# Kernel tuning notes

Measured on AMD Instinct MI355X. Metric: run time of the kernel, lower is better.

Reference implementation:

```python
import jax, jax.numpy as jnp
import numpy as np

N_NODES = 50000
N_EDGES = 800000
K_HOPS = 3


def setup_inputs() -> dict:
    key = jax.random.key(0)
    ks = jax.random.split(key, 8)
    x = jax.random.normal(ks[0], (N_NODES, 56), dtype=jnp.float32)
    edge_index = jax.random.randint(ks[1], (2, N_EDGES), 0, N_NODES, dtype=jnp.int64)
    def glorot(k, shape):
        fan_in, fan_out = shape
        s = (6.0 / (fan_in + fan_out)) ** 0.5
        return jax.random.uniform(k, shape, jnp.float32, -s, s)
    return {
        "x": x,
        "edge_index": edge_index,
        "W1": glorot(ks[2], (56, 64)), "b1": jnp.zeros((64,), jnp.float32),
        "W2": glorot(ks[3], (64, 64)), "b2": jnp.zeros((64,), jnp.float32),
        "W3": glorot(ks[4], (64, 64)), "b3": jnp.zeros((64,), jnp.float32),
        "W4": glorot(ks[5], (64, 256)), "b4": jnp.zeros((256,), jnp.float32),
    }


def _gcn_norm(edge_index, num_nodes, dtype):
    # add self loops (PyG SGConv default), then symmetric D^{-1/2}(A+I)D^{-1/2} weights
    loop = jnp.arange(num_nodes, dtype=edge_index.dtype)
    src = jnp.concatenate([edge_index[0], loop])
    dst = jnp.concatenate([edge_index[1], loop])
    deg = jax.ops.segment_sum(jnp.ones_like(src, dtype=dtype), dst, num_segments=num_nodes)
    dinv = jnp.where(deg > 0, jax.lax.rsqrt(deg), 0.0).astype(dtype)
    norm = dinv[src] * dinv[dst]  # [E + N]
    return src, dst, norm


def _propagate_k(h, src, dst, norm, num_nodes, k):
    # k hops of sparse gather-scale-scatter: h <- A_hat @ h
    for _ in range(k):
        h = jax.ops.segment_sum(h[src] * norm[:, None], dst, num_segments=num_nodes)
    return h


def reference(x, edge_index, W1, b1, W2, b2, W3, b3, W4, b4):
    n = x.shape[0]
    src, dst, norm = _gcn_norm(edge_index, n, x.dtype)
    # SGConv layers (dropout is identity in eval mode)
    h = _propagate_k(x, src, dst, norm, n, K_HOPS) @ W1 + b1
    h = _propagate_k(h, src, dst, norm, n, K_HOPS) @ W2 + b2
    h = _propagate_k(h, src, dst, norm, n, K_HOPS) @ W3 + b3
    return h @ W4 + b4  # [N, output]
```

## Files before the change

### kernel.cpp

```cpp
#include <hip/hip_runtime.h>

#define N_NODES 50000
#define N_EDGES 800000
#define N_GROUPS 12500
#define HALF_G 6250
#define GSLOTS 128
#define F_IN 56
#define F_PAD 64
#define F_OUT 256
#define NB 16
#define SEG_SZ 6250
#define ZROW N_NODES
#define PAD_E 0x7FFFFFFF


__global__ __launch_bounds__(256) void k_fill(const int* __restrict__ ei,
                                              int* __restrict__ gcnt,
                                              int* __restrict__ ellg) {
  int seg = blockIdx.x & 7;
  int chunk = blockIdx.x >> 3;
  int nchunks = gridDim.x >> 3;
  int stride = nchunks * blockDim.x;
  for (int e = chunk * blockDim.x + threadIdx.x; e < N_EDGES; e += stride) {
    int d = ei[N_EDGES + e];
    if (d / SEG_SZ == seg) {
      int s = ei[e];
      int g = d >> 2;
      int pos = atomicAdd(&gcnt[g], 1);
      ellg[(g << 7) + pos] = (s << 2) | (d & 3);
    }
  }
}


__global__ void k_self(int* __restrict__ gcnt, int* __restrict__ ellg) {
  int i = blockIdx.x * blockDim.x + threadIdx.x;
  if (i >= N_NODES) return;
  int g = i >> 2;
  int pos = atomicAdd(&gcnt[g], 1);
  ellg[(g << 7) + pos] = (i << 2) | (i & 3);
}


__global__ __launch_bounds__(256) void k_sort(const int* __restrict__ gcnt,
                                              int* __restrict__ ellg,
                                              float* __restrict__ dinv,
                                              float* __restrict__ ideg,
                                              float* __restrict__ sqd) {
  int w = (blockIdx.x * blockDim.x + threadIdx.x) >> 6;
  int l = threadIdx.x & 63;
  int cnt = __builtin_amdgcn_readfirstlane(gcnt[w]);
  int* base = ellg + ((size_t)w << 7);
  int v0 = (l < cnt) ? base[l] : PAD_E;
  int v1 = (64 + l < cnt) ? base[64 + l] : PAD_E;

#pragma unroll
  for (int k = 2; k <= 128; k <<= 1) {
#pragma unroll
    for (int j = 64; j > 0; j >>= 1) {
      if (j >= k) continue;
      if (j == 64) {
        int lo = min(v0, v1), hi = max(v0, v1);
        v0 = lo; v1 = hi;
      } else {
        int o0 = __shfl_xor(v0, j);
        int o1 = __shfl_xor(v1, j);
        bool lower = ((l & j) == 0);
        bool up0 = ((l & k) == 0);
        bool up1 = (((l + 64) & k) == 0);
        v0 = (lower == up0) ? min(v0, o0) : max(v0, o0);
        v1 = (lower == up1) ? min(v1, o1) : max(v1, o1);
      }
    }
  }

  int c0 = __popcll(__ballot(v0 != PAD_E && (v0 & 3) == 0)) +
           __popcll(__ballot(v1 != PAD_E && (v1 & 3) == 0));
  int c1 = __popcll(__ballot(v0 != PAD_E && (v0 & 3) == 1)) +
           __popcll(__ballot(v1 != PAD_E && (v1 & 3) == 1));
  int c2 = __popcll(__ballot(v0 != PAD_E && (v0 & 3) == 2)) +
           __popcll(__ballot(v1 != PAD_E && (v1 & 3) == 2));
  int c3 = __popcll(__ballot(v0 != PAD_E && (v0 & 3) == 3)) +
           __popcll(__ballot(v1 != PAD_E && (v1 & 3) == 3));
  if (l < 4) {
    int c = (l == 0) ? c0 : (l == 1) ? c1 : (l == 2) ? c2 : c3;
    float fc = (float)c;
    int node = (w << 2) + l;
    dinv[node] = rsqrtf(fc);
    ideg[node] = 1.0f / fc;
    sqd[node]  = sqrtf(fc);
  }

  base[l] = (v0 == PAD_E) ? (ZROW << 2) : v0;
  base[64 + l] = (v1 == PAD_E) ? (ZROW << 2) : v1;
}


__global__ void k_loadx(const float* __restrict__ x, const float* __restrict__ dinv,
                        float* __restrict__ h) {
  int i = blockIdx.x * blockDim.x + threadIdx.x;
  int nn = i >> 6, f = i & 63;
  float di = dinv[nn];
  float v = 0.f;
  if (f < F_IN) v = x[nn * F_IN + f] * di;
  else if (f == F_IN) v = di;
  h[i] = v;
}


template<bool ASC>
__device__ __forceinline__ void hop_group(int g, const float* __restrict__ hin,
                                          float* __restrict__ hout,
                                          const int* __restrict__ gcnt,
                                          const int* __restrict__ ellg,
                                          const float* __restrict__ ideg,
                                          float* __restrict__ vsave,
                                          int lane, int sub, int m, int fo) {
  int cnt = __builtin_amdgcn_readfirstlane(gcnt[g]);
  const int* base = ellg + ((size_t)g << 7);
  int rec0 = base[lane];
  int rec1 = base[64 + lane];
  float4 acc0 = make_float4(0.f, 0.f, 0.f, 0.f);
  float4 acc1 = acc0, acc2 = acc0, acc3 = acc0;
  int nq = (cnt + 3) >> 2;

#define GATHER(QI, EV, AV)                                                \
  int idx_##EV = ((QI) << 2) + sub;                                       \
  int EV = (idx_##EV < 64) ? __shfl(rec0, idx_##EV)                       \
                           : __shfl(rec1, idx_##EV - 64);                 \
  float4 AV = *(const float4*)(hin + (((size_t)(EV >> 2)) << 6) + fo);

#define ACCUM(EV, AV) {                                                   \
    int dd = EV & 3;                                                      \
    float m0 = (dd == 0) ? 1.f : 0.f;                                     \
    float m1 = (dd == 1) ? 1.f : 0.f;                                     \
    float m2 = (dd == 2) ? 1.f : 0.f;                                     \
    float m3 = (dd == 3) ? 1.f : 0.f;                                     \
    acc0.x = fmaf(m0, AV.x, acc0.x); acc0.y = fmaf(m0, AV.y, acc0.y);     \
    acc0.z = fmaf(m0, AV.z, acc0.z); acc0.w = fmaf(m0, AV.w, acc0.w);     \
    acc1.x = fmaf(m1, AV.x, acc1.x); acc1.y = fmaf(m1, AV.y, acc1.y);     \
    acc1.z = fmaf(m1, AV.z, acc1.z); acc1.w = fmaf(m1, AV.w, acc1.w);     \
    acc2.x = fmaf(m2, AV.x, acc2.x); acc2.y = fmaf(m2, AV.y, acc2.y);     \
    acc2.z = fmaf(m2, AV.z, acc2.z); acc2.w = fmaf(m2, AV.w, acc2.w);     \
    acc3.x = fmaf(m3, AV.x, acc3.x); acc3.y = fmaf(m3, AV.y, acc3.y);     \
    acc3.z = fmaf(m3, AV.z, acc3.z); acc3.w = fmaf(m3, AV.w, acc3.w);     \
  }

  int it = 0;
  for (; it + 2 <= nq; it += 2) {
    int q0 = ASC ? it : (nq - 1 - it);
    int q1 = ASC ? (it + 1) : (nq - 2 - it);
    GATHER(q0, e0, a0)
    GATHER(q1, e1, a1)
    ACCUM(e0, a0)
    ACCUM(e1, a1)
  }
  if (it < nq) {
    int q0 = ASC ? it : (nq - 1 - it);
    GATHER(q0, e0, a0)
    ACCUM(e0, a0)
  }
#undef GATHER
#undef ACCUM

#define RED(A) \
  A.x += __shfl_xor(A.x, 16); A.y += __shfl_xor(A.y, 16); \
  A.z += __shfl_xor(A.z, 16); A.w += __shfl_xor(A.w, 16); \
  A.x += __shfl_xor(A.x, 32); A.y += __shfl_xor(A.y, 32); \
  A.z += __shfl_xor(A.z, 32); A.w += __shfl_xor(A.w, 32);
  RED(acc0) RED(acc1) RED(acc2) RED(acc3)
#undef RED

  float4 v = (sub == 0) ? acc0 : (sub == 1) ? acc1 : (sub == 2) ? acc2 : acc3;
  int node = (g << 2) + sub;
  float idg = ideg[node];
  v.x *= idg; v.y *= idg; v.z *= idg; v.w *= idg;
  *(float4*)(hout + (((size_t)node) << 6) + fo) = v;
  if (vsave != nullptr && m == 14) vsave[node] = v.x;
}

__global__ __launch_bounds__(256) void k_hop(const float* __restrict__ hin,
                                             float* __restrict__ hout,
                                             const int* __restrict__ gcnt,
                                             const int* __restrict__ ellg,
                                             const float* __restrict__ ideg,
                                             float* __restrict__ vsave) {
  int wid = (blockIdx.x * blockDim.x + threadIdx.x) >> 6;
  int lane = threadIdx.x & 63;
  if (wid >= HALF_G) return;
  int sub = lane >> 4, m = lane & 15, fo = m << 2;
  hop_group<true >(wid, hin, hout, gcnt, ellg, ideg, vsave, lane, sub, m, fo);
  hop_group<false>(wid + HALF_G, hin, hout, gcnt, ellg, ideg, vsave, lane, sub, m, fo);
}


__global__ void k_weights(const float* __restrict__ W1, const float* __restrict__ b1,
                          const float* __restrict__ W2, const float* __restrict__ b2,
                          const float* __restrict__ W3, const float* __restrict__ b3,
                          const float* __restrict__ W4, const float* __restrict__ b4,
                          float* __restrict__ Mw, float* __restrict__ c1,
                          float* __restrict__ c2, float* __restrict__ c3) {
  __shared__ float t1[64], t2[64], t3[64];
  int m = blockIdx.x, tid = threadIdx.x;
  if (m < F_IN) {
    if (tid < 64) {
      float a = 0.f;
      for (int k = 0; k < 64; ++k) a = fmaf(W1[m * 64 + k], W2[k * 64 + tid], a);
      t1[tid] = a;
    }
    __syncthreads();
    if (tid < 64) {
      float a = 0.f;
      for (int k = 0; k < 64; ++k) a = fmaf(t1[k], W3[k * 64 + tid], a);
      t2[tid] = a;
    }
    __syncthreads();
    {
      float a = 0.f;
      for (int k = 0; k < 64; ++k) a = fmaf(t2[k], W4[k * 256 + tid], a);
      Mw[m * 256 + tid] = a;
    }
  } else {
    if (tid < 64) {
      float a = 0.f;
      for (int k = 0; k < 64; ++k) a = fmaf(b1[k], W2[k * 64 + tid], a);
      t1[tid] = a;
    }
    __syncthreads();
    if (tid < 64) {
      float a = 0.f, b = 0.f;
      for (int k = 0; k < 64; ++k) {
        float w3 = W3[k * 64 + tid];
        a = fmaf(t1[k], w3, a);
        b = fmaf(b2[k], w3, b);
      }
      t2[tid] = a; t3[tid] = b;
    }
    __syncthreads();
    {
      float a = 0.f, b = 0.f, c = 0.f;
      for (int k = 0; k < 64; ++k) {
        float w4 = W4[k * 256 + tid];
        a = fmaf(t2[k], w4, a);
        b = fmaf(t3[k], w4, b);
        c = fmaf(b3[k], w4, c);
      }
      c1[tid] = a; c2[tid] = b; c3[tid] = c + b4[tid];
    }
  }
}


__global__ __launch_bounds__(256) void k_final(const float* __restrict__ y,
                                               const float* __restrict__ v3u,
                                               const float* __restrict__ v6u,
                                               const float* __restrict__ sqd,
                                               const float* __restrict__ Mw,
                                               const float* __restrict__ c1,
                                               const float* __restrict__ c2,
                                               const float* __restrict__ c3,
                                               float* __restrict__ out) {
  __shared__ float4 yl[NB][16];
  __shared__ float v3l[NB], v6l[NB];
  int tid = threadIdx.x;
  int j = tid;

  float4 Mreg[14];
#pragma unroll
  for (int k4 = 0; k4 < 14; ++k4) {
    Mreg[k4].x = Mw[(k4 * 4 + 0) * F_OUT + j];
    Mreg[k4].y = Mw[(k4 * 4 + 1) * F_OUT + j];
    Mreg[k4].z = Mw[(k4 * 4 + 2) * F_OUT + j];
    Mreg[k4].w = Mw[(k4 * 4 + 3) * F_OUT + j];
  }
  float C1 = c1[j], C2 = c2[j], C3 = c3[j];

  int n0 = blockIdx.x * NB;
  {
    int i = tid;
    int nn = i >> 4, q = i & 15;
    float sq = sqd[n0 + nn];
    float4 v = *(const float4*)(y + ((size_t)(n0 + nn) << 6) + q * 4);
    v.x *= sq; v.y *= sq; v.z *= sq; v.w *= sq;
    yl[nn][q] = v;
  }
  if (tid < NB) {
    float sq = sqd[n0 + tid];
    v3l[tid] = v3u[n0 + tid] * sq;
    v6l[tid] = v6u[n0 + tid] * sq;
  }
  __syncthreads();

  float acc[NB];
#pragma unroll
  for (int nn = 0; nn < NB; ++nn)
    acc[nn] = fmaf(v6l[nn], C1, fmaf(v3l[nn], C2, C3));

#pragma unroll
  for (int k4 = 0; k4 < 14; ++k4) {
    float4 mk = Mreg[k4];
#pragma unroll
    for (int nn = 0; nn < NB; ++nn) {
      float4 yv = yl[nn][k4];
      acc[nn] = fmaf(yv.w, mk.w,
                fmaf(yv.z, mk.z,
                fmaf(yv.y, mk.y,
                fmaf(yv.x, mk.x, acc[nn]))));
    }
  }

#pragma unroll
  for (int nn = 0; nn < NB; ++nn)
    out[(size_t)(n0 + nn) * F_OUT + j] = acc[nn];
}


extern "C" void kernel_launch(void* const* d_in, const int* in_sizes, int n_in,
                              void* d_out, int out_size, void* d_ws, size_t ws_size,
                              hipStream_t stream) {
  const float* x  = (const float*)d_in[0];
  const int*   ei = (const int*)d_in[1];
  const float* W1 = (const float*)d_in[2];
  const float* b1 = (const float*)d_in[3];
  const float* W2 = (const float*)d_in[4];
  const float* b2 = (const float*)d_in[5];
  const float* W3 = (const float*)d_in[6];
  const float* b3 = (const float*)d_in[7];
  const float* W4 = (const float*)d_in[8];
  const float* b4 = (const float*)d_in[9];
  float* out = (float*)d_out;

  char* ws = (char*)d_ws;
  size_t off = 0;
  auto take = [&](size_t bytes) -> void* {
    void* p = ws + off;
    off += (bytes + 255) & ~(size_t)255;
    return p;
  };
  int*   gcnt  = (int*)take((size_t)N_GROUPS * 4);
  float* dinv  = (float*)take((size_t)N_NODES * 4);
  float* ideg  = (float*)take((size_t)N_NODES * 4);
  float* sqd   = (float*)take((size_t)N_NODES * 4);
  float* v3    = (float*)take((size_t)N_NODES * 4);
  float* v6    = (float*)take((size_t)N_NODES * 4);
  int*   ellg  = (int*)take((size_t)N_GROUPS * GSLOTS * 4);
  float* hA    = (float*)take((size_t)(N_NODES + 1) * F_PAD * 4);
  float* hB    = (float*)take((size_t)(N_NODES + 1) * F_PAD * 4);
  float* Mw    = (float*)take((size_t)F_IN * F_OUT * 4);
  float* c1    = (float*)take((size_t)F_OUT * 4);
  float* c2    = (float*)take((size_t)F_OUT * 4);
  float* c3    = (float*)take((size_t)F_OUT * 4);

  (void)hipMemsetAsync(gcnt, 0, (size_t)N_GROUPS * 4, stream);
  (void)hipMemsetAsync(hA + (size_t)ZROW * F_PAD, 0, F_PAD * 4, stream);
  (void)hipMemsetAsync(hB + (size_t)ZROW * F_PAD, 0, F_PAD * 4, stream);
  k_fill<<<1024, 256, 0, stream>>>(ei, gcnt, ellg);
  k_self<<<(N_NODES + 255) / 256, 256, 0, stream>>>(gcnt, ellg);
  k_sort<<<(N_GROUPS * 64) / 256, 256, 0, stream>>>(gcnt, ellg, dinv, ideg, sqd);
  k_loadx<<<(N_NODES * F_PAD) / 256, 256, 0, stream>>>(x, dinv, hA);
  k_weights<<<F_IN + 1, 256, 0, stream>>>(W1, b1, W2, b2, W3, b3, W4, b4, Mw, c1, c2, c3);

  int hop_blocks = (HALF_G * 64 + 255) / 256;
  float* src = hA;
  float* dst = hB;
  for (int hop = 1; hop <= 9; ++hop) {
    float* vs = (hop == 3) ? v3 : (hop == 6) ? v6 : nullptr;
    k_hop<<<hop_blocks, 256, 0, stream>>>(src, dst, gcnt, ellg, ideg, vs);
    float* t = src; src = dst; dst = t;
  }
  k_final<<<N_NODES / NB, 256, 0, stream>>>(src, v3, v6, sqd, Mw, c1, c2, c3, out);
}
```

Measured before the change: 351.0 us.

## Fold self-loops into sort, use fixed-length hop loops, add nontemporal memory ops

```diff
diff --git a/kernel.cpp b/kernel.cpp
--- a/kernel.cpp
+++ b/kernel.cpp
@@ -13,6 +13,8 @@
 #define ZROW N_NODES
 #define PAD_E 0x7FFFFFFF
 
+typedef float f32x4 __attribute__((ext_vector_type(4)));
+
 
 __global__ __launch_bounds__(256) void k_fill(const int* __restrict__ ei,
                                               int* __restrict__ gcnt,
@@ -22,23 +24,14 @@
   int nchunks = gridDim.x >> 3;
   int stride = nchunks * blockDim.x;
   for (int e = chunk * blockDim.x + threadIdx.x; e < N_EDGES; e += stride) {
-    int d = ei[N_EDGES + e];
+    int d = __builtin_nontemporal_load(ei + N_EDGES + e);
     if (d / SEG_SZ == seg) {
-      int s = ei[e];
+      int s = __builtin_nontemporal_load(ei + e);
       int g = d >> 2;
       int pos = atomicAdd(&gcnt[g], 1);
       ellg[(g << 7) + pos] = (s << 2) | (d & 3);
     }
   }
-}
-
-
-__global__ void k_self(int* __restrict__ gcnt, int* __restrict__ ellg) {
-  int i = blockIdx.x * blockDim.x + threadIdx.x;
-  if (i >= N_NODES) return;
-  int g = i >> 2;
-  int pos = atomicAdd(&gcnt[g], 1);
-  ellg[(g << 7) + pos] = (i << 2) | (i & 3);
 }
 
 
@@ -50,9 +43,13 @@
   int w = (blockIdx.x * blockDim.x + threadIdx.x) >> 6;
   int l = threadIdx.x & 63;
   int cnt = __builtin_amdgcn_readfirstlane(gcnt[w]);
+  int tot = cnt + 4;
   int* base = ellg + ((size_t)w << 7);
-  int v0 = (l < cnt) ? base[l] : PAD_E;
-  int v1 = (64 + l < cnt) ? base[64 + l] : PAD_E;
+  int i0 = l, i1 = 64 + l;
+  int v0 = (i0 < cnt) ? base[i0]
+         : (i0 < tot) ? ((((w << 2) + (i0 - cnt)) << 2) | (i0 - cnt)) : PAD_E;
+  int v1 = (i1 < cnt) ? base[i1]
+         : (i1 < tot) ? ((((w << 2) + (i1 - cnt)) << 2) | (i1 - cnt)) : PAD_E;
 
 #pragma unroll
   for (int k = 2; k <= 128; k <<= 1) {
@@ -91,7 +88,7 @@
     sqd[node]  = sqrtf(fc);
   }
 
-  base[l] = (v0 == PAD_E) ? (ZROW << 2) : v0;
+  base[l]      = (v0 == PAD_E) ? (ZROW << 2) : v0;
   base[64 + l] = (v1 == PAD_E) ? (ZROW << 2) : v1;
 }
 
@@ -108,26 +105,8 @@
 }
 
 
-template<bool ASC>
-__device__ __forceinline__ void hop_group(int g, const float* __restrict__ hin,
-                                          float* __restrict__ hout,
-                                          const int* __restrict__ gcnt,
-                                          const int* __restrict__ ellg,
-                                          const float* __restrict__ ideg,
-                                          float* __restrict__ vsave,
-                                          int lane, int sub, int m, int fo) {
-  int cnt = __builtin_amdgcn_readfirstlane(gcnt[g]);
-  const int* base = ellg + ((size_t)g << 7);
-  int rec0 = base[lane];
-  int rec1 = base[64 + lane];
-  float4 acc0 = make_float4(0.f, 0.f, 0.f, 0.f);
-  float4 acc1 = acc0, acc2 = acc0, acc3 = acc0;
-  int nq = (cnt + 3) >> 2;
-
-#define GATHER(QI, EV, AV)                                                \
-  int idx_##EV = ((QI) << 2) + sub;                                       \
-  int EV = (idx_##EV < 64) ? __shfl(rec0, idx_##EV)                       \
-                           : __shfl(rec1, idx_##EV - 64);                 \
+#define GATHER(REC, IQ, EV, AV)                                           \
+  int EV = __shfl(REC, IQ);                                               \
   float4 AV = *(const float4*)(hin + (((size_t)(EV >> 2)) << 6) + fo);
 
 #define ACCUM(EV, AV) {                                                   \
@@ -146,22 +125,41 @@
     acc3.z = fmaf(m3, AV.z, acc3.z); acc3.w = fmaf(m3, AV.w, acc3.w);     \
   }
 
-  int it = 0;
-  for (; it + 2 <= nq; it += 2) {
-    int q0 = ASC ? it : (nq - 1 - it);
-    int q1 = ASC ? (it + 1) : (nq - 2 - it);
-    GATHER(q0, e0, a0)
-    GATHER(q1, e1, a1)
-    ACCUM(e0, a0)
-    ACCUM(e1, a1)
-  }
-  if (it < nq) {
-    int q0 = ASC ? it : (nq - 1 - it);
-    GATHER(q0, e0, a0)
-    ACCUM(e0, a0)
-  }
-#undef GATHER
-#undef ACCUM
+template<bool ASC>
+__device__ __forceinline__ void hop_group(int g, const float* __restrict__ hin,
+                                          float* __restrict__ hout,
+                                          const int* __restrict__ ellg,
+                                          const float* __restrict__ ideg,
+                                          float* __restrict__ vsave,
+                                          int lane, int sub, int m, int fo) {
+  const int* base = ellg + ((size_t)g << 7);
+  int rec0 = __builtin_nontemporal_load(base + lane);
+  int rec1 = __builtin_nontemporal_load(base + 64 + lane);
+  float4 acc0 = make_float4(0.f, 0.f, 0.f, 0.f);
+  float4 acc1 = acc0, acc2 = acc0, acc3 = acc0;
+
+#pragma unroll 1
+  for (int it = 0; it < 4; ++it) {
+    int qb = ASC ? (it << 2) : (28 - (it << 2));
+    int rA = ASC ? rec0 : rec1;
+    int iq = (ASC ? (qb << 2) : ((qb - 16) << 2)) + sub;
+    GATHER(rA, iq,      e0, a0)
+    GATHER(rA, iq + 4,  e1, a1)
+    GATHER(rA, iq + 8,  e2, a2)
+    GATHER(rA, iq + 12, e3, a3)
+    ACCUM(e0, a0) ACCUM(e1, a1) ACCUM(e2, a2) ACCUM(e3, a3)
+  }
+#pragma unroll 1
+  for (int it = 0; it < 4; ++it) {
+    int qb = ASC ? (16 + (it << 2)) : (12 - (it << 2));
+    int rA = ASC ? rec1 : rec0;
+    int iq = (ASC ? ((qb - 16) << 2) : (qb << 2)) + sub;
+    GATHER(rA, iq,      e0, a0)
+    GATHER(rA, iq + 4,  e1, a1)
+    GATHER(rA, iq + 8,  e2, a2)
+    GATHER(rA, iq + 12, e3, a3)
+    ACCUM(e0, a0) ACCUM(e1, a1) ACCUM(e2, a2) ACCUM(e3, a3)
+  }
 
 #define RED(A) \
   A.x += __shfl_xor(A.x, 16); A.y += __shfl_xor(A.y, 16); \
@@ -181,7 +179,6 @@
 
 __global__ __launch_bounds__(256) void k_hop(const float* __restrict__ hin,
                                              float* __restrict__ hout,
-                                             const int* __restrict__ gcnt,
                                              const int* __restrict__ ellg,
                                              const float* __restrict__ ideg,
                                              float* __restrict__ vsave) {
@@ -189,8 +186,8 @@
   int lane = threadIdx.x & 63;
   if (wid >= HALF_G) return;
   int sub = lane >> 4, m = lane & 15, fo = m << 2;
-  hop_group<true >(wid, hin, hout, gcnt, ellg, ideg, vsave, lane, sub, m, fo);
-  hop_group<false>(wid + HALF_G, hin, hout, gcnt, ellg, ideg, vsave, lane, sub, m, fo);
+  hop_group<true >(wid, hin, hout, ellg, ideg, vsave, lane, sub, m, fo);
+  hop_group<false>(wid + HALF_G, hin, hout, ellg, ideg, vsave, lane, sub, m, fo);
 }
 
 
@@ -280,8 +277,9 @@
     int i = tid;
     int nn = i >> 4, q = i & 15;
     float sq = sqd[n0 + nn];
-    float4 v = *(const float4*)(y + ((size_t)(n0 + nn) << 6) + q * 4);
-    v.x *= sq; v.y *= sq; v.z *= sq; v.w *= sq;
+    f32x4 vv = __builtin_nontemporal_load(
+        (const f32x4*)(y + ((size_t)(n0 + nn) << 6) + q * 4));
+    float4 v; v.x = vv.x * sq; v.y = vv.y * sq; v.z = vv.z * sq; v.w = vv.w * sq;
     yl[nn][q] = v;
   }
   if (tid < NB) {
@@ -311,7 +309,7 @@
 
 #pragma unroll
   for (int nn = 0; nn < NB; ++nn)
-    out[(size_t)(n0 + nn) * F_OUT + j] = acc[nn];
+    __builtin_nontemporal_store(acc[nn], out + (size_t)(n0 + nn) * F_OUT + j);
 }
 
 
@@ -355,7 +353,6 @@
   (void)hipMemsetAsync(hA + (size_t)ZROW * F_PAD, 0, F_PAD * 4, stream);
   (void)hipMemsetAsync(hB + (size_t)ZROW * F_PAD, 0, F_PAD * 4, stream);
   k_fill<<<1024, 256, 0, stream>>>(ei, gcnt, ellg);
-  k_self<<<(N_NODES + 255) / 256, 256, 0, stream>>>(gcnt, ellg);
   k_sort<<<(N_GROUPS * 64) / 256, 256, 0, stream>>>(gcnt, ellg, dinv, ideg, sqd);
   k_loadx<<<(N_NODES * F_PAD) / 256, 256, 0, stream>>>(x, dinv, hA);
   k_weights<<<F_IN + 1, 256, 0, stream>>>(W1, b1, W2, b2, W3, b3, W4, b4, Mw, c1, c2, c3);
@@ -365,7 +362,7 @@
   float* dst = hB;
   for (int hop = 1; hop <= 9; ++hop) {
     float* vs = (hop == 3) ? v3 : (hop == 6) ? v6 : nullptr;
-    k_hop<<<hop_blocks, 256, 0, stream>>>(src, dst, gcnt, ellg, ideg, vs);
+    k_hop<<<hop_blocks, 256, 0, stream>>>(src, dst, ellg, ideg, vs);
     float* t = src; src = dst; dst = t;
   }
   k_final<<<N_NODES / NB, 256, 0, stream>>>(src, v3, v6, sqd, Mw, c1, c2, c3, out);
```

Result: slower. 392.4 us (+11.8%).

## Fold self-loops into sort, one group per wave, unroll gathers by eight

Applied to the files above, without the earlier changes.

```diff
diff --git a/kernel.cpp b/kernel.cpp
--- a/kernel.cpp
+++ b/kernel.cpp
@@ -3,7 +3,6 @@
 #define N_NODES 50000
 #define N_EDGES 800000
 #define N_GROUPS 12500
-#define HALF_G 6250
 #define GSLOTS 128
 #define F_IN 56
 #define F_PAD 64
@@ -12,6 +11,8 @@
 #define SEG_SZ 6250
 #define ZROW N_NODES
 #define PAD_E 0x7FFFFFFF
+
+typedef float f32x4 __attribute__((ext_vector_type(4)));
 
 
 __global__ __launch_bounds__(256) void k_fill(const int* __restrict__ ei,
@@ -33,15 +34,6 @@
 }
 
 
-__global__ void k_self(int* __restrict__ gcnt, int* __restrict__ ellg) {
-  int i = blockIdx.x * blockDim.x + threadIdx.x;
-  if (i >= N_NODES) return;
-  int g = i >> 2;
-  int pos = atomicAdd(&gcnt[g], 1);
-  ellg[(g << 7) + pos] = (i << 2) | (i & 3);
-}
-
-
 __global__ __launch_bounds__(256) void k_sort(const int* __restrict__ gcnt,
                                               int* __restrict__ ellg,
                                               float* __restrict__ dinv,
@@ -50,9 +42,13 @@
   int w = (blockIdx.x * blockDim.x + threadIdx.x) >> 6;
   int l = threadIdx.x & 63;
   int cnt = __builtin_amdgcn_readfirstlane(gcnt[w]);
+  int tot = cnt + 4;
   int* base = ellg + ((size_t)w << 7);
-  int v0 = (l < cnt) ? base[l] : PAD_E;
-  int v1 = (64 + l < cnt) ? base[64 + l] : PAD_E;
+  int i0 = l, i1 = 64 + l;
+  int v0 = (i0 < cnt) ? base[i0]
+         : (i0 < tot) ? ((((w << 2) + (i0 - cnt)) << 2) | (i0 - cnt)) : PAD_E;
+  int v1 = (i1 < cnt) ? base[i1]
+         : (i1 < tot) ? ((((w << 2) + (i1 - cnt)) << 2) | (i1 - cnt)) : PAD_E;
 
 #pragma unroll
   for (int k = 2; k <= 128; k <<= 1) {
@@ -91,7 +87,7 @@
     sqd[node]  = sqrtf(fc);
   }
 
-  base[l] = (v0 == PAD_E) ? (ZROW << 2) : v0;
+  base[l]      = (v0 == PAD_E) ? (ZROW << 2) : v0;
   base[64 + l] = (v1 == PAD_E) ? (ZROW << 2) : v1;
 }
 
@@ -108,26 +104,26 @@
 }
 
 
-template<bool ASC>
-__device__ __forceinline__ void hop_group(int g, const float* __restrict__ hin,
-                                          float* __restrict__ hout,
-                                          const int* __restrict__ gcnt,
-                                          const int* __restrict__ ellg,
-                                          const float* __restrict__ ideg,
-                                          float* __restrict__ vsave,
-                                          int lane, int sub, int m, int fo) {
+__global__ __launch_bounds__(256) void k_hop(const float* __restrict__ hin,
+                                             float* __restrict__ hout,
+                                             const int* __restrict__ gcnt,
+                                             const int* __restrict__ ellg,
+                                             const float* __restrict__ ideg,
+                                             float* __restrict__ vsave) {
+  int g = (blockIdx.x * blockDim.x + threadIdx.x) >> 6;
+  int lane = threadIdx.x & 63;
+  int sub = lane >> 4, m = lane & 15, fo = m << 2;
   int cnt = __builtin_amdgcn_readfirstlane(gcnt[g]);
+  int nq = (cnt + 7) >> 2;
   const int* base = ellg + ((size_t)g << 7);
   int rec0 = base[lane];
   int rec1 = base[64 + lane];
   float4 acc0 = make_float4(0.f, 0.f, 0.f, 0.f);
   float4 acc1 = acc0, acc2 = acc0, acc3 = acc0;
-  int nq = (cnt + 3) >> 2;
-
-#define GATHER(QI, EV, AV)                                                \
-  int idx_##EV = ((QI) << 2) + sub;                                       \
-  int EV = (idx_##EV < 64) ? __shfl(rec0, idx_##EV)                       \
-                           : __shfl(rec1, idx_##EV - 64);                 \
+
+#define GQ(Q, EV, AV)                                                     \
+  int r_##EV = ((Q) < 16) ? rec0 : rec1;                                  \
+  int EV = __shfl(r_##EV, (((Q) & 15) << 2) + sub);                       \
   float4 AV = *(const float4*)(hin + (((size_t)(EV >> 2)) << 6) + fo);
 
 #define ACCUM(EV, AV) {                                                   \
@@ -146,21 +142,29 @@
     acc3.z = fmaf(m3, AV.z, acc3.z); acc3.w = fmaf(m3, AV.w, acc3.w);     \
   }
 
-  int it = 0;
-  for (; it + 2 <= nq; it += 2) {
-    int q0 = ASC ? it : (nq - 1 - it);
-    int q1 = ASC ? (it + 1) : (nq - 2 - it);
-    GATHER(q0, e0, a0)
-    GATHER(q1, e1, a1)
+  int q = 0;
+  for (; q + 8 <= nq; q += 8) {
+    GQ(q + 0, e0, a0)
+    GQ(q + 1, e1, a1)
+    GQ(q + 2, e2, a2)
+    GQ(q + 3, e3, a3)
+    GQ(q + 4, e4, a4)
+    GQ(q + 5, e5, a5)
+    GQ(q + 6, e6, a6)
+    GQ(q + 7, e7, a7)
+    ACCUM(e0, a0) ACCUM(e1, a1) ACCUM(e2, a2) ACCUM(e3, a3)
+    ACCUM(e4, a4) ACCUM(e5, a5) ACCUM(e6, a6) ACCUM(e7, a7)
+  }
+  for (; q + 2 <= nq; q += 2) {
+    GQ(q + 0, e0, a0)
+    GQ(q + 1, e1, a1)
+    ACCUM(e0, a0) ACCUM(e1, a1)
+  }
+  if (q < nq) {
+    GQ(q, e0, a0)
     ACCUM(e0, a0)
-    ACCUM(e1, a1)
-  }
-  if (it < nq) {
-    int q0 = ASC ? it : (nq - 1 - it);
-    GATHER(q0, e0, a0)
-    ACCUM(e0, a0)
-  }
-#undef GATHER
+  }
+#undef GQ
 #undef ACCUM
 
 #define RED(A) \
@@ -177,20 +181,6 @@
   v.x *= idg; v.y *= idg; v.z *= idg; v.w *= idg;
   *(float4*)(hout + (((size_t)node) << 6) + fo) = v;
   if (vsave != nullptr && m == 14) vsave[node] = v.x;
-}
-
-__global__ __launch_bounds__(256) void k_hop(const float* __restrict__ hin,
-                                             float* __restrict__ hout,
-                                             const int* __restrict__ gcnt,
-                                             const int* __restrict__ ellg,
-                                             const float* __restrict__ ideg,
-                                             float* __restrict__ vsave) {
-  int wid = (blockIdx.x * blockDim.x + threadIdx.x) >> 6;
-  int lane = threadIdx.x & 63;
-  if (wid >= HALF_G) return;
-  int sub = lane >> 4, m = lane & 15, fo = m << 2;
-  hop_group<true >(wid, hin, hout, gcnt, ellg, ideg, vsave, lane, sub, m, fo);
-  hop_group<false>(wid + HALF_G, hin, hout, gcnt, ellg, ideg, vsave, lane, sub, m, fo);
 }
 
 
@@ -355,17 +345,15 @@
   (void)hipMemsetAsync(hA + (size_t)ZROW * F_PAD, 0, F_PAD * 4, stream);
   (void)hipMemsetAsync(hB + (size_t)ZROW * F_PAD, 0, F_PAD * 4, stream);
   k_fill<<<1024, 256, 0, stream>>>(ei, gcnt, ellg);
-  k_self<<<(N_NODES + 255) / 256, 256, 0, stream>>>(gcnt, ellg);
   k_sort<<<(N_GROUPS * 64) / 256, 256, 0, stream>>>(gcnt, ellg, dinv, ideg, sqd);
   k_loadx<<<(N_NODES * F_PAD) / 256, 256, 0, stream>>>(x, dinv, hA);
   k_weights<<<F_IN + 1, 256, 0, stream>>>(W1, b1, W2, b2, W3, b3, W4, b4, Mw, c1, c2, c3);
 
-  int hop_blocks = (HALF_G * 64 + 255) / 256;
   float* src = hA;
   float* dst = hB;
   for (int hop = 1; hop <= 9; ++hop) {
     float* vs = (hop == 3) ? v3 : (hop == 6) ? v6 : nullptr;
-    k_hop<<<hop_blocks, 256, 0, stream>>>(src, dst, gcnt, ellg, ideg, vs);
+    k_hop<<<(N_GROUPS * 64) / 256, 256, 0, stream>>>(src, dst, gcnt, ellg, ideg, vs);
     float* t = src; src = dst; dst = t;
   }
   k_final<<<N_NODES / NB, 256, 0, stream>>>(src, v3, v6, sqd, Mw, c1, c2, c3, out);
```

New measurement: 339.8 us. 3.2% less time.
